# Optimization experiments

Measured on AMD Instinct MI355X. Metric: run time of the kernel, lower is better.

Reference implementation:

```python
import jax, jax.numpy as jnp
import numpy as np

B, V = 256, 128000

def setup_inputs() -> dict:
    key = jax.random.key(0)
    k1, k2 = jax.random.split(key)
    logits = jax.random.normal(k1, (B, V), dtype=jnp.float32)
    temperatures = jax.random.uniform(k2, (B,), dtype=jnp.float32)
    return {"logits": logits, "temperatures": temperatures}

def reference(logits, temperatures):
    # temperature-scaled probs (float32), temp==0 treated as 1 for the divide
    logits_f = logits.astype(jnp.float32)
    safe_t = jnp.where(temperatures == 0, jnp.ones_like(temperatures), temperatures)
    scaled = logits_f / safe_t[:, None]                      # [B, V]
    probs = jax.nn.softmax(scaled, axis=-1)                  # [B, V] fp32
    # greedy tokens from the ORIGINAL logits (torch in-place div only touched the copy)
    greedy_tokens = jnp.argmax(logits_f, axis=-1)            # [B] int
    # multinomial sampling == Gumbel-max / categorical over scaled logits
    sample_key = jax.random.key(42)
    sampled_tokens = jax.random.categorical(sample_key, scaled, axis=-1)  # [B]
    tokens = jnp.where(temperatures == 0, greedy_tokens, sampled_tokens)
    return tokens, probs
```

## Files before the change

kernel.cpp:

```cpp
#include <hip/hip_runtime.h>
#include <cstdint>
#include <cmath>

#define B_ROWS 256
#define V_COLS 128000
#define CHUNKS 25
#define CHUNK_QUADS 1280
#define ATHREADS 256
#define AWAVES 4
#define QPT 5
#define ELEMS_PT 20
#define LN2F 0.69314718055994530942f

#define G_STRIDE 4
#define FIN_OFF (B_ROWS * CHUNKS * G_STRIDE)
#define S_OFF (FIN_OFF + B_ROWS * 4)

__device__ __forceinline__ uint32_t rotl32(uint32_t x, uint32_t d) {
  return __builtin_amdgcn_alignbit(x, x, 32u - d);
}

__device__ __forceinline__ uint32_t threefry_xor(uint32_t x0, uint32_t x1) {
  const uint32_t k0 = 0u;
  const uint32_t k1 = 42u;
  const uint32_t k2 = 0x1BD11BDAu ^ k0 ^ k1;
  x0 += k0; x1 += k1;
#define TF_RND(r) { x0 += x1; x1 = rotl32(x1, (r)); x1 ^= x0; }
  TF_RND(13) TF_RND(15) TF_RND(26) TF_RND(6)
  x0 += k1; x1 += k2 + 1u;
  TF_RND(17) TF_RND(29) TF_RND(16) TF_RND(24)
  x0 += k2; x1 += k0 + 2u;
  TF_RND(13) TF_RND(15) TF_RND(26) TF_RND(6)
  x0 += k0; x1 += k1 + 3u;
  TF_RND(17) TF_RND(29) TF_RND(16) TF_RND(24)
  x0 += k1; x1 += k2 + 4u;
  TF_RND(13) TF_RND(15) TF_RND(26) TF_RND(6)
  x0 += k2; x1 += k0 + 5u;
#undef TF_RND
  return x0 ^ x1;
}

__device__ __forceinline__ float gumbel_l2(uint32_t bits) {
  uint32_t ub = (bits >> 9) | 0x3f800000u;
  float f = __uint_as_float(ub) - 1.0f;
  float u = fmaxf(f, 1.17549435e-38f);
  const float l1 = __log2f(u);
  const float nl = -LN2F * l1;
  return __log2f(nl);
}

__global__ __launch_bounds__(ATHREADS, 4) void pass1_kernel(
    const float* __restrict__ logits,
    const float* __restrict__ temps,
    float* __restrict__ ws) {
  const uint32_t bx = blockIdx.x;
  const uint32_t b = bx / CHUNKS;
  const uint32_t chunk = bx - b * CHUNKS;
  const int tid = threadIdx.x;
  const float t = temps[b];
  const float inv_t = (t == 0.0f) ? 1.0f : (1.0f / t);
  const float* __restrict__ row = logits + (size_t)b * V_COLS;
  const int q0 = (int)chunk * CHUNK_QUADS + tid;

  float4 xq[QPT];
#pragma unroll
  for (int j = 0; j < QPT; ++j)
    xq[j] = reinterpret_cast<const float4*>(row)[q0 + j * ATHREADS];

  float sx[ELEMS_PT];
#pragma unroll
  for (int j = 0; j < QPT; ++j) {
    sx[4 * j + 0] = xq[j].x * inv_t;
    sx[4 * j + 1] = xq[j].y * inv_t;
    sx[4 * j + 2] = xq[j].z * inv_t;
    sx[4 * j + 3] = xq[j].w * inv_t;
  }

  float mthr = sx[0];
#pragma unroll
  for (int k = 1; k < ELEMS_PT; ++k) mthr = fmaxf(mthr, sx[k]);
  float s = 0.0f;
#pragma unroll
  for (int k = 0; k < ELEMS_PT; ++k) s += __expf(sx[k] - mthr);

  float av = -INFINITY; int ai = 0;
  const int v0 = q0 * 4;
#pragma unroll
  for (int j = 0; j < QPT; ++j) {
    const float xa[4] = {xq[j].x, xq[j].y, xq[j].z, xq[j].w};
#pragma unroll
    for (int k = 0; k < 4; ++k) {
      const bool up = xa[k] > av;
      av = up ? xa[k] : av;
      ai = up ? (v0 + j * 1024 + k) : ai;
    }
  }

  float m = mthr;
#pragma unroll
  for (int off = 32; off > 0; off >>= 1) {
    float ov = __shfl_xor(av, off);
    int   oi = __shfl_xor(ai, off);
    if (ov > av || (ov == av && oi < ai)) { av = ov; ai = oi; }
    float om = __shfl_xor(m, off);
    float os = __shfl_xor(s, off);
    float mn = fmaxf(m, om);
    s = fmaf(s, __expf(m - mn), os * __expf(om - mn));
    m = mn;
  }

  __shared__ float lds_av[AWAVES]; __shared__ int lds_ai[AWAVES];
  __shared__ float lds_m[AWAVES];  __shared__ float lds_s[AWAVES];
  const int wid = tid >> 6;
  if ((tid & 63) == 0) {
    lds_av[wid] = av; lds_ai[wid] = ai;
    lds_m[wid] = m;   lds_s[wid] = s;
  }
  __syncthreads();
  if (tid == 0) {
    float Av = lds_av[0]; int Ai = lds_ai[0];
    float M = lds_m[0];   float S = lds_s[0];
#pragma unroll
    for (int w = 1; w < AWAVES; ++w) {
      float ov = lds_av[w]; int oi = lds_ai[w];
      if (ov > Av || (ov == Av && oi < Ai)) { Av = ov; Ai = oi; }
      float om = lds_m[w]; float os = lds_s[w];
      float mn = fmaxf(M, om);
      S = fmaf(S, __expf(M - mn), os * __expf(om - mn));
      M = mn;
    }
    float* p = ws + (size_t)(b * CHUNKS + chunk) * G_STRIDE;
    p[0] = Av; p[1] = __int_as_float(Ai);
    p[2] = M;  p[3] = S;
  }
}

__global__ __launch_bounds__(B_ROWS) void fin1_kernel(
    float* __restrict__ ws) {
  const int r = threadIdx.x;
  const float* p = ws + (size_t)r * CHUNKS * G_STRIDE;
  float Av = -INFINITY; int Ai = 0;
  float M = -INFINITY;  float S = 0.0f;
#pragma unroll
  for (int c = 0; c < CHUNKS; ++c) {
    const float* q = p + c * G_STRIDE;
    float ov = q[0]; int oi = __float_as_int(q[1]);
    if (ov > Av) { Av = ov; Ai = oi; }
    float om = q[2]; float os = q[3];
    float mn = fmaxf(M, om);
    S = fmaf(S, __expf(M - mn), os * __expf(om - mn));
    M = mn;
  }
  float* f = ws + FIN_OFF + 4 * r;
  f[0] = M;
  f[1] = 1.0f / S;
  f[2] = __int_as_float(Ai);
}

__global__ __launch_bounds__(ATHREADS, 4) void pass2_kernel(
    const float* __restrict__ logits,
    const float* __restrict__ temps,
    float* __restrict__ ws,
    float* __restrict__ out) {
  const uint32_t bx = blockIdx.x;
  const uint32_t b = bx / CHUNKS;
  const uint32_t chunk = bx - b * CHUNKS;
  const int tid = threadIdx.x;
  const float t = temps[b];
  const float inv_t = (t == 0.0f) ? 1.0f : (1.0f / t);
  const float M = ws[FIN_OFF + 4 * b + 0];
  const float invS = ws[FIN_OFF + 4 * b + 1];
  const float* __restrict__ row = logits + (size_t)b * V_COLS;
  float* __restrict__ prow = out + B_ROWS + (size_t)b * V_COLS;
  const int q0 = (int)chunk * CHUNK_QUADS + tid;

  float4 xq[QPT];
#pragma unroll
  for (int j = 0; j < QPT; ++j)
    xq[j] = reinterpret_cast<const float4*>(row)[q0 + j * ATHREADS];

#pragma unroll
  for (int j = 0; j < QPT; ++j) {
    float4 p4;
    p4.x = __expf(fmaf(xq[j].x, inv_t, -M)) * invS;
    p4.y = __expf(fmaf(xq[j].y, inv_t, -M)) * invS;
    p4.z = __expf(fmaf(xq[j].z, inv_t, -M)) * invS;
    p4.w = __expf(fmaf(xq[j].w, inv_t, -M)) * invS;
    reinterpret_cast<float4*>(prow)[q0 + j * ATHREADS] = p4;
  }

  float av = -INFINITY; int ai = 0;
  if (t != 0.0f) {
    const int v0 = q0 * 4;
    const uint32_t cb = b * (uint32_t)V_COLS + (uint32_t)v0;
#pragma unroll
    for (int j = 0; j < QPT; ++j) {
      const float xa[4] = {xq[j].x, xq[j].y, xq[j].z, xq[j].w};
#pragma unroll
      for (int k = 0; k < 4; ++k) {
        const float sxv = xa[k] * inv_t;
        const float c = fmaf(-LN2F,
            gumbel_l2(threefry_xor(0u, cb + (uint32_t)(j * 1024 + k))), sxv);
        const bool up = c > av;
        av = up ? c : av;
        ai = up ? (v0 + j * 1024 + k) : ai;
      }
    }
  }

#pragma unroll
  for (int off = 32; off > 0; off >>= 1) {
    float ov = __shfl_xor(av, off);
    int   oi = __shfl_xor(ai, off);
    if (ov > av || (ov == av && oi < ai)) { av = ov; ai = oi; }
  }

  __shared__ float lds_av[AWAVES]; __shared__ int lds_ai[AWAVES];
  const int wid = tid >> 6;
  if ((tid & 63) == 0) { lds_av[wid] = av; lds_ai[wid] = ai; }
  __syncthreads();
  if (tid == 0) {
    float Av = lds_av[0]; int Ai = lds_ai[0];
#pragma unroll
    for (int w = 1; w < AWAVES; ++w) {
      float ov = lds_av[w]; int oi = lds_ai[w];
      if (ov > Av || (ov == Av && oi < Ai)) { Av = ov; Ai = oi; }
    }
    float* p = ws + S_OFF + (size_t)(b * CHUNKS + chunk) * 2;
    p[0] = Av; p[1] = __int_as_float(Ai);
  }
}

__global__ __launch_bounds__(B_ROWS) void fin2_kernel(
    const float* __restrict__ temps,
    const float* __restrict__ ws,
    float* __restrict__ out) {
  const int r = threadIdx.x;
  const float t = temps[r];
  int token;
  if (t == 0.0f) {
    token = __float_as_int(ws[FIN_OFF + 4 * r + 2]);
  } else {
    const float* p = ws + S_OFF + (size_t)r * CHUNKS * 2;
    float Sv = -INFINITY; int Si = 0;
#pragma unroll
    for (int c = 0; c < CHUNKS; ++c) {
      float ov = p[2 * c]; int oi = __float_as_int(p[2 * c + 1]);
      if (ov > Sv) { Sv = ov; Si = oi; }
    }
    token = Si;
  }
  out[r] = (float)token;
}

extern "C" void kernel_launch(void* const* d_in, const int* in_sizes, int n_in,
                              void* d_out, int out_size, void* d_ws, size_t ws_size,
                              hipStream_t stream) {
  const float* logits = (const float*)d_in[0];
  const float* temps  = (const float*)d_in[1];
  float* out = (float*)d_out;
  float* ws  = (float*)d_ws;
  pass1_kernel<<<B_ROWS * CHUNKS, ATHREADS, 0, stream>>>(logits, temps, ws);
  fin1_kernel<<<1, B_ROWS, 0, stream>>>(ws);
  pass2_kernel<<<B_ROWS * CHUNKS, ATHREADS, 0, stream>>>(logits, temps, ws, out);
  fin2_kernel<<<1, B_ROWS, 0, stream>>>(temps, ws, out);
}
```

Measured before the change: 110.5 us.

## Split Gumbel sampling work between pass1 and pass2 by chunk

Moves the Threefry/Gumbel argmax for the first 13 chunks of each row into pass1, leaving pass2 to handle only the remaining chunks. This balances the compute-heavy RNG work across both passes, so each pass is less ALU-bound relative to its memory traffic. It also uses the per-thread greedy max (scaled) as the softmax shift instead of a separate max loop. The __syncthreads inside a block-uniform branch in pass2 is safe. Using av*inv_t as the max is only exact for positive temperatures.

```diff
diff --git a/kernel.cpp b/kernel.cpp
--- a/kernel.cpp
+++ b/kernel.cpp
@@ -5,6 +5,7 @@
 #define B_ROWS 256
 #define V_COLS 128000
 #define CHUNKS 25
+#define GSPLIT 13
 #define CHUNK_QUADS 1280
 #define ATHREADS 256
 #define AWAVES 4
@@ -76,13 +77,6 @@
     sx[4 * j + 3] = xq[j].w * inv_t;
   }
 
-  float mthr = sx[0];
-#pragma unroll
-  for (int k = 1; k < ELEMS_PT; ++k) mthr = fmaxf(mthr, sx[k]);
-  float s = 0.0f;
-#pragma unroll
-  for (int k = 0; k < ELEMS_PT; ++k) s += __expf(sx[k] - mthr);
-
   float av = -INFINITY; int ai = 0;
   const int v0 = q0 * 4;
 #pragma unroll
@@ -96,12 +90,38 @@
     }
   }
 
+  const float mthr = av * inv_t;
+  float s = 0.0f;
+#pragma unroll
+  for (int k = 0; k < ELEMS_PT; ++k) s += __expf(sx[k] - mthr);
+
+  float gv = -INFINITY; int gi = 0;
+  const bool do_gumbel = (chunk < GSPLIT) && (t != 0.0f);
+  if (do_gumbel) {
+    const uint32_t cb = b * (uint32_t)V_COLS + (uint32_t)v0;
+#pragma unroll
+    for (int j = 0; j < QPT; ++j) {
+#pragma unroll
+      for (int k = 0; k < 4; ++k) {
+        const float c = fmaf(-LN2F,
+            gumbel_l2(threefry_xor(0u, cb + (uint32_t)(j * 1024 + k))),
+            sx[4 * j + k]);
+        const bool up = c > gv;
+        gv = up ? c : gv;
+        gi = up ? (v0 + j * 1024 + k) : gi;
+      }
+    }
+  }
+
   float m = mthr;
 #pragma unroll
   for (int off = 32; off > 0; off >>= 1) {
     float ov = __shfl_xor(av, off);
     int   oi = __shfl_xor(ai, off);
     if (ov > av || (ov == av && oi < ai)) { av = ov; ai = oi; }
+    float o2v = __shfl_xor(gv, off);
+    int   o2i = __shfl_xor(gi, off);
+    if (o2v > gv || (o2v == gv && o2i < gi)) { gv = o2v; gi = o2i; }
     float om = __shfl_xor(m, off);
     float os = __shfl_xor(s, off);
     float mn = fmaxf(m, om);
@@ -110,20 +130,25 @@
   }
 
   __shared__ float lds_av[AWAVES]; __shared__ int lds_ai[AWAVES];
+  __shared__ float lds_gv[AWAVES]; __shared__ int lds_gi[AWAVES];
   __shared__ float lds_m[AWAVES];  __shared__ float lds_s[AWAVES];
   const int wid = tid >> 6;
   if ((tid & 63) == 0) {
     lds_av[wid] = av; lds_ai[wid] = ai;
+    lds_gv[wid] = gv; lds_gi[wid] = gi;
     lds_m[wid] = m;   lds_s[wid] = s;
   }
   __syncthreads();
   if (tid == 0) {
     float Av = lds_av[0]; int Ai = lds_ai[0];
+    float Gv = lds_gv[0]; int Gi = lds_gi[0];
     float M = lds_m[0];   float S = lds_s[0];
 #pragma unroll
     for (int w = 1; w < AWAVES; ++w) {
       float ov = lds_av[w]; int oi = lds_ai[w];
       if (ov > Av || (ov == Av && oi < Ai)) { Av = ov; Ai = oi; }
+      float o2v = lds_gv[w]; int o2i = lds_gi[w];
+      if (o2v > Gv || (o2v == Gv && o2i < Gi)) { Gv = o2v; Gi = o2i; }
       float om = lds_m[w]; float os = lds_s[w];
       float mn = fmaxf(M, om);
       S = fmaf(S, __expf(M - mn), os * __expf(om - mn));
@@ -132,6 +157,10 @@
     float* p = ws + (size_t)(b * CHUNKS + chunk) * G_STRIDE;
     p[0] = Av; p[1] = __int_as_float(Ai);
     p[2] = M;  p[3] = S;
+    if (do_gumbel) {
+      float* q = ws + S_OFF + (size_t)(b * CHUNKS + chunk) * 2;
+      q[0] = Gv; q[1] = __int_as_float(Gi);
+    }
   }
 }
 
@@ -189,8 +218,9 @@
     reinterpret_cast<float4*>(prow)[q0 + j * ATHREADS] = p4;
   }
 
-  float av = -INFINITY; int ai = 0;
-  if (t != 0.0f) {
+  const bool do_gumbel = (chunk >= GSPLIT) && (t != 0.0f);
+  float gv = -INFINITY; int gi = 0;
+  if (do_gumbel) {
     const int v0 = q0 * 4;
     const uint32_t cb = b * (uint32_t)V_COLS + (uint32_t)v0;
 #pragma unroll
@@ -201,33 +231,33 @@
         const float sxv = xa[k] * inv_t;
         const float c = fmaf(-LN2F,
             gumbel_l2(threefry_xor(0u, cb + (uint32_t)(j * 1024 + k))), sxv);
-        const bool up = c > av;
-        av = up ? c : av;
-        ai = up ? (v0 + j * 1024 + k) : ai;
+        const bool up = c > gv;
+        gv = up ? c : gv;
+        gi = up ? (v0 + j * 1024 + k) : gi;
       }
     }
-  }
-
-#pragma unroll
-  for (int off = 32; off > 0; off >>= 1) {
-    float ov = __shfl_xor(av, off);
-    int   oi = __shfl_xor(ai, off);
-    if (ov > av || (ov == av && oi < ai)) { av = ov; ai = oi; }
-  }
-
-  __shared__ float lds_av[AWAVES]; __shared__ int lds_ai[AWAVES];
-  const int wid = tid >> 6;
-  if ((tid & 63) == 0) { lds_av[wid] = av; lds_ai[wid] = ai; }
-  __syncthreads();
-  if (tid == 0) {
-    float Av = lds_av[0]; int Ai = lds_ai[0];
-#pragma unroll
-    for (int w = 1; w < AWAVES; ++w) {
-      float ov = lds_av[w]; int oi = lds_ai[w];
-      if (ov > Av || (ov == Av && oi < Ai)) { Av = ov; Ai = oi; }
-    }
-    float* p = ws + S_OFF + (size_t)(b * CHUNKS + chunk) * 2;
-    p[0] = Av; p[1] = __int_as_float(Ai);
+
+#pragma unroll
+    for (int off = 32; off > 0; off >>= 1) {
+      float ov = __shfl_xor(gv, off);
+      int   oi = __shfl_xor(gi, off);
+      if (ov > gv || (ov == gv && oi < gi)) { gv = ov; gi = oi; }
+    }
+
+    __shared__ float lds_gv[AWAVES]; __shared__ int lds_gi[AWAVES];
+    const int wid = tid >> 6;
+    if ((tid & 63) == 0) { lds_gv[wid] = gv; lds_gi[wid] = gi; }
+    __syncthreads();
+    if (tid == 0) {
+      float Gv = lds_gv[0]; int Gi = lds_gi[0];
+#pragma unroll
+      for (int w = 1; w < AWAVES; ++w) {
+        float ov = lds_gv[w]; int oi = lds_gi[w];
+        if (ov > Gv || (ov == Gv && oi < Gi)) { Gv = ov; Gi = oi; }
+      }
+      float* p = ws + S_OFF + (size_t)(b * CHUNKS + chunk) * 2;
+      p[0] = Gv; p[1] = __int_as_float(Gi);
+    }
   }
 }
 
```

Result: slower. 117.1 us (+6.0%).

## Skip Gumbel noise for logits outside the bounded sampling window

Applied to the files above, without the earlier changes.

In the sampling pass, each group of four logits gets the threefry plus Gumbel work only if some lane's scaled max lies within a fixed window below the row max. Because the Gumbel noise drawn from a 23-bit uniform is bounded, tokens outside that window cannot win, so the expensive RNG and log math is skipped for almost all elements. The pass also skips the whole reduction for temperature-zero rows and folds the key constants into the threefry input. Pass 1 now takes the scaled max from the raw argmax instead of a separate max loop, which assumes a positive inverse temperature. Wave-level branching adds some divergence overhead in return.

```diff
diff --git a/kernel.cpp b/kernel.cpp
--- a/kernel.cpp
+++ b/kernel.cpp
@@ -11,6 +11,7 @@
 #define QPT 5
 #define ELEMS_PT 20
 #define LN2F 0.69314718055994530942f
+#define GUMBEL_WINDOW 21.2f
 
 #define G_STRIDE 4
 #define FIN_OFF (B_ROWS * CHUNKS * G_STRIDE)
@@ -20,22 +21,21 @@
   return __builtin_amdgcn_alignbit(x, x, 32u - d);
 }
 
-__device__ __forceinline__ uint32_t threefry_xor(uint32_t x0, uint32_t x1) {
-  const uint32_t k0 = 0u;
+__device__ __forceinline__ uint32_t threefry_xor_pre(uint32_t x1) {
   const uint32_t k1 = 42u;
-  const uint32_t k2 = 0x1BD11BDAu ^ k0 ^ k1;
-  x0 += k0; x1 += k1;
+  const uint32_t k2 = 0x1BD11BF0u;
+  uint32_t x0 = 0u;
 #define TF_RND(r) { x0 += x1; x1 = rotl32(x1, (r)); x1 ^= x0; }
   TF_RND(13) TF_RND(15) TF_RND(26) TF_RND(6)
   x0 += k1; x1 += k2 + 1u;
   TF_RND(17) TF_RND(29) TF_RND(16) TF_RND(24)
-  x0 += k2; x1 += k0 + 2u;
+  x0 += k2; x1 += 0u + 2u;
   TF_RND(13) TF_RND(15) TF_RND(26) TF_RND(6)
-  x0 += k0; x1 += k1 + 3u;
+  x0 += 0u; x1 += k1 + 3u;
   TF_RND(17) TF_RND(29) TF_RND(16) TF_RND(24)
   x0 += k1; x1 += k2 + 4u;
   TF_RND(13) TF_RND(15) TF_RND(26) TF_RND(6)
-  x0 += k2; x1 += k0 + 5u;
+  x0 += k2; x1 += 0u + 5u;
 #undef TF_RND
   return x0 ^ x1;
 }
@@ -67,22 +67,6 @@
   for (int j = 0; j < QPT; ++j)
     xq[j] = reinterpret_cast<const float4*>(row)[q0 + j * ATHREADS];
 
-  float sx[ELEMS_PT];
-#pragma unroll
-  for (int j = 0; j < QPT; ++j) {
-    sx[4 * j + 0] = xq[j].x * inv_t;
-    sx[4 * j + 1] = xq[j].y * inv_t;
-    sx[4 * j + 2] = xq[j].z * inv_t;
-    sx[4 * j + 3] = xq[j].w * inv_t;
-  }
-
-  float mthr = sx[0];
-#pragma unroll
-  for (int k = 1; k < ELEMS_PT; ++k) mthr = fmaxf(mthr, sx[k]);
-  float s = 0.0f;
-#pragma unroll
-  for (int k = 0; k < ELEMS_PT; ++k) s += __expf(sx[k] - mthr);
-
   float av = -INFINITY; int ai = 0;
   const int v0 = q0 * 4;
 #pragma unroll
@@ -94,6 +78,16 @@
       av = up ? xa[k] : av;
       ai = up ? (v0 + j * 1024 + k) : ai;
     }
+  }
+
+  const float mthr = av * inv_t;
+  float s = 0.0f;
+#pragma unroll
+  for (int j = 0; j < QPT; ++j) {
+    s += __expf(fmaf(xq[j].x, inv_t, -mthr));
+    s += __expf(fmaf(xq[j].y, inv_t, -mthr));
+    s += __expf(fmaf(xq[j].z, inv_t, -mthr));
+    s += __expf(fmaf(xq[j].w, inv_t, -mthr));
   }
 
   float m = mthr;
@@ -189,45 +183,50 @@
     reinterpret_cast<float4*>(prow)[q0 + j * ATHREADS] = p4;
   }
 
-  float av = -INFINITY; int ai = 0;
+  float gv = -INFINITY; int gi = 0;
   if (t != 0.0f) {
     const int v0 = q0 * 4;
-    const uint32_t cb = b * (uint32_t)V_COLS + (uint32_t)v0;
+    const uint32_t cb42 = b * (uint32_t)V_COLS + (uint32_t)v0 + 42u;
+    const float thrM = M - GUMBEL_WINDOW;
 #pragma unroll
     for (int j = 0; j < QPT; ++j) {
       const float xa[4] = {xq[j].x, xq[j].y, xq[j].z, xq[j].w};
-#pragma unroll
-      for (int k = 0; k < 4; ++k) {
-        const float sxv = xa[k] * inv_t;
-        const float c = fmaf(-LN2F,
-            gumbel_l2(threefry_xor(0u, cb + (uint32_t)(j * 1024 + k))), sxv);
-        const bool up = c > av;
-        av = up ? c : av;
-        ai = up ? (v0 + j * 1024 + k) : ai;
+      const float mx4 = fmaxf(fmaxf(xa[0], xa[1]), fmaxf(xa[2], xa[3]));
+      if (__any(mx4 * inv_t > thrM)) {
+#pragma unroll
+        for (int k = 0; k < 4; ++k) {
+          const float sxv = xa[k] * inv_t;
+          const float c = fmaf(-LN2F,
+              gumbel_l2(threefry_xor_pre(cb42 + (uint32_t)(j * 1024 + k))),
+              sxv);
+          const bool up = c > gv;
+          gv = up ? c : gv;
+          gi = up ? (v0 + j * 1024 + k) : gi;
+        }
       }
     }
-  }
-
-#pragma unroll
-  for (int off = 32; off > 0; off >>= 1) {
-    float ov = __shfl_xor(av, off);
-    int   oi = __shfl_xor(ai, off);
-    if (ov > av || (ov == av && oi < ai)) { av = ov; ai = oi; }
-  }
-
-  __shared__ float lds_av[AWAVES]; __shared__ int lds_ai[AWAVES];
-  const int wid = tid >> 6;
-  if ((tid & 63) == 0) { lds_av[wid] = av; lds_ai[wid] = ai; }
-  __syncthreads();
-  if (tid == 0) {
-    float Av = lds_av[0]; int Ai = lds_ai[0];
-#pragma unroll
-    for (int w = 1; w < AWAVES; ++w) {
-      float ov = lds_av[w]; int oi = lds_ai[w];
-      if (ov > Av || (ov == Av && oi < Ai)) { Av = ov; Ai = oi; }
-    }
-    float* p = ws + S_OFF + (size_t)(b * CHUNKS + chunk) * 2;
-    p[0] = Av; p[1] = __int_as_float(Ai);
+
+#pragma unroll
+    for (int off = 32; off > 0; off >>= 1) {
+      float ov = __shfl_xor(gv, off);
+      int   oi = __shfl_xor(gi, off);
+      if (ov > gv || (ov == gv && oi < gi)) { gv = ov; gi = oi; }
+    }
+
+    __shared__ float lds_gv[AWAVES]; __shared__ int lds_gi[AWAVES];
+    const int wid = tid >> 6;
+    if ((tid & 63) == 0) { lds_gv[wid] = gv; lds_gi[wid] = gi; }
+    __syncthreads();
+    if (tid == 0) {
+      float Gv = lds_gv[0]; int Gi = lds_gi[0];
+#pragma unroll
+      for (int w = 1; w < AWAVES; ++w) {
+        float ov = lds_gv[w]; int oi = lds_gi[w];
+        if (ov > Gv || (ov == Gv && oi < Gi)) { Gv = ov; Gi = oi; }
+      }
+      float* p = ws + S_OFF + (size_t)(b * CHUNKS + chunk) * 2;
+      p[0] = Gv; p[1] = __int_as_float(Gi);
+    }
   }
 }
 
```

Result: faster. 106.4 us (-3.7%).
